# Kernel optimization log

Hardware: AMD Instinct MI355X
Metric: run time of the kernel (lower is better)

Reference implementation:

```python
import jax, jax.numpy as jnp
import numpy as np

N, T, F, H = 50000, 8, 128, 128
E = 800000


def setup_inputs() -> dict:
    key = jax.random.key(0)
    ks = jax.random.split(key, 10)
    s = 1.0 / np.sqrt(H)
    return {
        "node_features": jax.random.normal(ks[0], (T, N, F), jnp.float32),
        "edge_index": jax.random.randint(ks[1], (T, 2, E), 0, N),
        "W1": jax.random.normal(ks[2], (F, H), jnp.float32) * s,
        "b1": jnp.zeros((H,), jnp.float32),
        "W2": jax.random.normal(ks[3], (H, H), jnp.float32) * s,
        "b2": jnp.zeros((H,), jnp.float32),
        "W_ih": jax.random.uniform(ks[4], (4 * H, H), jnp.float32, -s, s),
        "W_hh": jax.random.uniform(ks[5], (4 * H, H), jnp.float32, -s, s),
        "b_ih": jax.random.uniform(ks[6], (4 * H,), jnp.float32, -s, s),
        "b_hh": jax.random.uniform(ks[7], (4 * H,), jnp.float32, -s, s),
    }


def gcn_layer(x, src, dst, W, b):
    """PyG GCNConv: add self loops, symmetric D^-1/2 (A+I) D^-1/2 normalization."""
    n = x.shape[0]
    h = x @ W  # [N, H]
    deg = jnp.zeros((n,), x.dtype).at[dst].add(1.0) + 1.0  # degree incl. self loop
    dinv = jax.lax.rsqrt(deg)
    norm = (dinv[src] * dinv[dst])[:, None]  # per-edge norm
    msg = h[src] * norm  # [E, H] gather + scale
    agg = jax.ops.segment_sum(msg, dst, num_segments=n)  # scatter-add at targets
    agg = agg + h * (dinv * dinv)[:, None]  # self-loop contribution
    return agg + b


def reference(node_features, edge_index, W1, b1, W2, b2, W_ih, W_hh, b_ih, b_hh):
    # per-timestep 2-layer GCN (dropout in eval mode -> identity)
    def step_gnn(_, xe):
        x, ei = xe
        src, dst = ei[0], ei[1]
        h = jax.nn.relu(gcn_layer(x, src, dst, W1, b1))
        h = jax.nn.relu(gcn_layer(h, src, dst, W2, b2))
        return None, h

    _, embs = jax.lax.scan(step_gnn, None, (node_features, edge_index))  # [T, N, H]

    # single-layer LSTM over T, batch dim = N; pytorch gate order i,f,g,o
    def lstm_step(carry, x_t):
        h, c = carry
        gates = x_t @ W_ih.T + h @ W_hh.T + b_ih + b_hh
        i, f, g, o = jnp.split(gates, 4, axis=-1)
        c = jax.nn.sigmoid(f) * c + jax.nn.sigmoid(i) * jnp.tanh(g)
        h = jax.nn.sigmoid(o) * jnp.tanh(c)
        return (h, c), None

    h0 = jnp.zeros((N, H), node_features.dtype)
    (h_last, _), _ = jax.lax.scan(lstm_step, (h0, h0), embs)
    return h_last  # [N, H] = lstm_out[:, -1, :]
```

## Files before the change

### kernel.cpp

```cpp
#include <hip/hip_runtime.h>
#include <cstdint>
#include <cstddef>

#define NN 50000
#define TT 8
#define FF 128
#define HH 128
#define EE 800000

#define NBUCK 782
#define NB 128
#define CHUNK 6250

typedef __attribute__((ext_vector_type(8))) short bf16x8;
typedef __attribute__((ext_vector_type(4))) float f32x4;
typedef unsigned int uint;
typedef unsigned short ushort;

__device__ __forceinline__ float sigmoidf(float x) { return 1.0f / (1.0f + expf(-x)); }

__device__ __forceinline__ ushort f2bf_rne(float x) {
    uint u = __float_as_uint(x);
    uint r = (u + 0x7FFFu + ((u >> 16) & 1u)) >> 16;
    return (ushort)r;
}
__device__ __forceinline__ float bf2f(ushort b) { return __uint_as_float(((uint)b) << 16); }
__device__ __forceinline__ void split1(float x, ushort& hi, ushort& lo) {
    ushort h = f2bf_rne(x);
    hi = h;
    lo = f2bf_rne(x - bf2f(h));
}


__global__ __launch_bounds__(256) void bin_hist(const int* __restrict__ ei,
                                                int* __restrict__ histG) {
    __shared__ int hist[NBUCK];
    const int tid = threadIdx.x;
    const int blk = blockIdx.x, t = blockIdx.y;
    for (int i = tid; i < NBUCK; i += 256) hist[i] = 0;
    __syncthreads();
    const int* dst = ei + (size_t)t * 2 * EE + EE;
    const int base = blk * CHUNK;
    for (int i = tid; i < CHUNK; i += 256) atomicAdd(&hist[dst[base + i] >> 6], 1);
    __syncthreads();
    int* hg = histG + (size_t)t * NBUCK * NB;
    for (int i = tid; i < NBUCK; i += 256) hg[i * NB + blk] = hist[i];
}

__global__ __launch_bounds__(256) void scan_bins(int* __restrict__ histG,
                                                 int* __restrict__ bOffs) {
    __shared__ int sums[256];
    const int t = blockIdx.x;
    int* hg = histG + (size_t)t * NBUCK * NB;
    int* bo = bOffs + (size_t)t * (NBUCK + 1);
    const int tid = threadIdx.x;
    const int SZ = NBUCK * NB;
    const int chunk = (SZ + 255) / 256;
    const int b = tid * chunk, e = min(b + chunk, SZ);
    int s = 0;
    for (int i = b; i < e; ++i) s += hg[i];
    sums[tid] = s;
    __syncthreads();
    for (int o = 1; o < 256; o <<= 1) {
        int v = 0;
        if (tid >= o) v = sums[tid - o];
        __syncthreads();
        if (tid >= o) sums[tid] += v;
        __syncthreads();
    }
    int pre = (tid == 0) ? 0 : sums[tid - 1];
    for (int i = b; i < e; ++i) {
        int v = hg[i];
        hg[i] = pre;
        if ((i & (NB - 1)) == 0) bo[i / NB] = pre;
        pre += v;
    }
    if (tid == 255) bo[NBUCK] = pre;
}

__global__ __launch_bounds__(256) void bin_scatter(const int* __restrict__ ei,
                                                   const int* __restrict__ histG,
                                                   uint* __restrict__ binned) {
    __shared__ int cur[NBUCK];
    const int tid = threadIdx.x;
    const int blk = blockIdx.x, t = blockIdx.y;
    const int* hg = histG + (size_t)t * NBUCK * NB;
    for (int i = tid; i < NBUCK; i += 256) cur[i] = hg[i * NB + blk];
    __syncthreads();
    const int* src = ei + (size_t)t * 2 * EE;
    const int* dst = src + EE;
    uint* bn = binned + (size_t)t * EE;
    const int base = blk * CHUNK;
    for (int i = tid; i < CHUNK; i += 256) {
        const int e = base + i;
        const int d = dst[e];
        const int s = src[e];
        const int pos = atomicAdd(&cur[d >> 6], 1);
        bn[pos] = ((uint)(d & 63) << 16) | (uint)s;
    }
}

__global__ __launch_bounds__(256) void bucket_csr(const uint* __restrict__ binned,
                                                  const int* __restrict__ bOffs,
                                                  int* __restrict__ sorted,
                                                  int* __restrict__ offs,
                                                  float* __restrict__ dinv) {
    __shared__ int cnt[64];
    __shared__ int base[64];
    const int tid = threadIdx.x;
    const int buck = blockIdx.x, t = blockIdx.y;
    if (tid < 64) cnt[tid] = 0;
    __syncthreads();
    const int* bo = bOffs + (size_t)t * (NBUCK + 1);
    const uint* bn = binned + (size_t)t * EE;
    const int e0 = bo[buck], e1 = bo[buck + 1];
    for (int e = e0 + tid; e < e1; e += 256) atomicAdd(&cnt[bn[e] >> 16], 1);
    __syncthreads();
    if (tid == 0) {
        int pre = e0;
#pragma unroll
        for (int i = 0; i < 64; ++i) { base[i] = pre; pre += cnt[i]; }
    }
    __syncthreads();
    if (tid < 64) {
        const int d = buck * 64 + tid;
        if (d < NN) {
            offs[(size_t)t * (NN + 1) + d] = base[tid];
            dinv[(size_t)t * NN + d] = rsqrtf((float)(cnt[tid] + 1));
        }
        cnt[tid] = 0;
    }
    __syncthreads();
    int* so = sorted + (size_t)t * EE;
    for (int e = e0 + tid; e < e1; e += 256) {
        const uint p = bn[e];
        const int dl = p >> 16;
        const int pos = base[dl] + atomicAdd(&cnt[dl], 1);
        so[pos] = (int)(p & 0xFFFF);
    }
    if (buck == 0 && tid == 0) offs[(size_t)t * (NN + 1) + NN] = EE;
}

__global__ void prep_w_gcn(const float* __restrict__ W, ushort* __restrict__ oh,
                           ushort* __restrict__ ol) {
    const int bx = blockIdx.x;
    const int kc5 = bx >> 3, q = bx & 7;
    const int l = threadIdx.x;
    const int n = q * 16 + (l & 15);
    const int kb = kc5 * 32 + (l >> 4) * 8;
    const size_t o = ((size_t)bx * 64 + l) * 8;
#pragma unroll
    for (int j = 0; j < 8; ++j) {
        float v = W[(size_t)(kb + j) * 128 + n];
        split1(v, oh[o + j], ol[o + j]);
    }
}

__global__ void prep_w_lstm(const float* __restrict__ W, ushort* __restrict__ oh,
                            ushort* __restrict__ ol) {
    const int bx = blockIdx.x;
    const int kc5 = bx >> 5, q = bx & 31;
    const int l = threadIdx.x;
    const int c15 = l & 15;
    const int g = q & 3, kk = q >> 2;
    const int srow = g * 128 + kk * 16 + c15;
    const int kb = kc5 * 32 + (l >> 4) * 8;
    const size_t o = ((size_t)bx * 64 + l) * 8;
#pragma unroll
    for (int j = 0; j < 8; ++j) {
        float v = W[(size_t)srow * 128 + kb + j];
        split1(v, oh[o + j], ol[o + j]);
    }
}

__global__ void prep_bc(const float* __restrict__ bih, const float* __restrict__ bhh,
                        float* __restrict__ bcp) {
    const int cp = threadIdx.x;
    const int c15 = cp & 15, q = cp >> 4;
    const int g = q & 3, kk = q >> 2;
    const int srow = g * 128 + kk * 16 + c15;
    bcp[cp] = bih[srow] + bhh[srow];
}

__global__ __launch_bounds__(256) void gemm_gcn_mfma(const float* __restrict__ A,
                                                     const ushort* __restrict__ Wfh,
                                                     const ushort* __restrict__ Wfl,
                                                     const float* __restrict__ dinv,
                                                     float* __restrict__ C, int M) {
    __shared__ ushort Ah[64][40];
    __shared__ ushort Al[64][40];
    const int tid = threadIdx.x;
    const int lane = tid & 63;
    const int w = tid >> 6;
    const int wm = w >> 1, wn = w & 1;
    const int l15 = lane & 15, l4 = lane >> 4;
    const int m0 = blockIdx.x * 64;

    f32x4 acc[2][4];
#pragma unroll
    for (int i = 0; i < 2; ++i)
#pragma unroll
        for (int j = 0; j < 4; ++j) acc[i][j] = (f32x4){0.f, 0.f, 0.f, 0.f};

    const int srow = tid >> 2;
    const int sseg = tid & 3;
    const bool aval = (m0 + srow) < M;
    const float* aptr = A + (size_t)(m0 + srow) * 128 + sseg * 8;

    for (int kc5 = 0; kc5 < 4; ++kc5) {
        float4 v0 = {0.f, 0.f, 0.f, 0.f}, v1 = {0.f, 0.f, 0.f, 0.f};
        if (aval) {
            v0 = *(const float4*)(aptr + kc5 * 32);
            v1 = *(const float4*)(aptr + kc5 * 32 + 4);
        }
        union { uint4 u; ushort s[8]; } ph, pl;
        split1(v0.x, ph.s[0], pl.s[0]); split1(v0.y, ph.s[1], pl.s[1]);
        split1(v0.z, ph.s[2], pl.s[2]); split1(v0.w, ph.s[3], pl.s[3]);
        split1(v1.x, ph.s[4], pl.s[4]); split1(v1.y, ph.s[5], pl.s[5]);
        split1(v1.z, ph.s[6], pl.s[6]); split1(v1.w, ph.s[7], pl.s[7]);
        *(uint4*)&Ah[srow][sseg * 8] = ph.u;
        *(uint4*)&Al[srow][sseg * 8] = pl.u;
        __syncthreads();

        bf16x8 bh[4], bl[4];
#pragma unroll
        for (int nf = 0; nf < 4; ++nf) {
            const size_t o = ((size_t)(kc5 * 8 + wn * 4 + nf) * 64 + lane) * 8;
            bh[nf] = *(const bf16x8*)(Wfh + o);
            bl[nf] = *(const bf16x8*)(Wfl + o);
        }
        bf16x8 ahf[2], alf[2];
#pragma unroll
        for (int mf = 0; mf < 2; ++mf) {
            ahf[mf] = *(const bf16x8*)&Ah[wm * 32 + mf * 16 + l15][l4 * 8];
            alf[mf] = *(const bf16x8*)&Al[wm * 32 + mf * 16 + l15][l4 * 8];
        }
#pragma unroll
        for (int mf = 0; mf < 2; ++mf)
#pragma unroll
            for (int nf = 0; nf < 4; ++nf) {
                acc[mf][nf] = __builtin_amdgcn_mfma_f32_16x16x32_bf16(ahf[mf], bh[nf], acc[mf][nf], 0, 0, 0);
                acc[mf][nf] = __builtin_amdgcn_mfma_f32_16x16x32_bf16(ahf[mf], bl[nf], acc[mf][nf], 0, 0, 0);
                acc[mf][nf] = __builtin_amdgcn_mfma_f32_16x16x32_bf16(alf[mf], bh[nf], acc[mf][nf], 0, 0, 0);
            }
        __syncthreads();
    }

#pragma unroll
    for (int mf = 0; mf < 2; ++mf)
#pragma unroll
        for (int r = 0; r < 4; ++r) {
            const int row = m0 + wm * 32 + mf * 16 + l4 * 4 + r;
            if (row < M) {
                const float d = dinv[row];
                float* cp = C + (size_t)row * 128 + wn * 64 + l15;
#pragma unroll
                for (int nf = 0; nf < 4; ++nf) cp[nf * 16] = acc[mf][nf][r] * d;
            }
        }
}

__global__ __launch_bounds__(256) void gemm_frag(const ushort* __restrict__ Xh,
                                                 const ushort* __restrict__ Xl,
                                                 const ushort* __restrict__ Wfh,
                                                 const ushort* __restrict__ Wfl,
                                                 const float* __restrict__ dinv,
                                                 float* __restrict__ C, int M) {
    const int tid = threadIdx.x;
    const int lane = tid & 63;
    const int w = tid >> 6;
    const int wm = w >> 1, wn = w & 1;
    const int l15 = lane & 15, l4 = lane >> 4;
    const int m0 = blockIdx.x * 64;

    f32x4 acc[2][4];
#pragma unroll
    for (int i = 0; i < 2; ++i)
#pragma unroll
        for (int j = 0; j < 4; ++j) acc[i][j] = (f32x4){0.f, 0.f, 0.f, 0.f};

    size_t abase[2];
#pragma unroll
    for (int mf = 0; mf < 2; ++mf)
        abase[mf] = (size_t)(m0 + wm * 32 + mf * 16 + l15) * 128 + l4 * 8;

#pragma unroll
    for (int kc5 = 0; kc5 < 4; ++kc5) {
        bf16x8 ahf[2], alf[2];
#pragma unroll
        for (int mf = 0; mf < 2; ++mf) {
            ahf[mf] = *(const bf16x8*)(Xh + abase[mf] + kc5 * 32);
            alf[mf] = *(const bf16x8*)(Xl + abase[mf] + kc5 * 32);
        }
#pragma unroll
        for (int nf = 0; nf < 4; ++nf) {
            const size_t o = ((size_t)(kc5 * 8 + wn * 4 + nf) * 64 + lane) * 8;
            const bf16x8 bh = *(const bf16x8*)(Wfh + o);
            const bf16x8 bl = *(const bf16x8*)(Wfl + o);
#pragma unroll
            for (int mf = 0; mf < 2; ++mf) {
                acc[mf][nf] = __builtin_amdgcn_mfma_f32_16x16x32_bf16(ahf[mf], bh, acc[mf][nf], 0, 0, 0);
                acc[mf][nf] = __builtin_amdgcn_mfma_f32_16x16x32_bf16(ahf[mf], bl, acc[mf][nf], 0, 0, 0);
                acc[mf][nf] = __builtin_amdgcn_mfma_f32_16x16x32_bf16(alf[mf], bh, acc[mf][nf], 0, 0, 0);
            }
        }
    }

#pragma unroll
    for (int mf = 0; mf < 2; ++mf)
#pragma unroll
        for (int r = 0; r < 4; ++r) {
            const int row = m0 + wm * 32 + mf * 16 + l4 * 4 + r;
            if (row < M) {
                const float d = dinv[row];
                float* cp = C + (size_t)row * 128 + wn * 64 + l15;
#pragma unroll
                for (int nf = 0; nf < 4; ++nf) cp[nf * 16] = acc[mf][nf][r] * d;
            }
        }
}

__global__ __launch_bounds__(256) void aggregate_q(const float* __restrict__ hs,
                                                   const int* __restrict__ offs,
                                                   const int* __restrict__ sorted,
                                                   const float* __restrict__ dinv,
                                                   const float* __restrict__ bias,
                                                   ushort* __restrict__ outh,
                                                   ushort* __restrict__ outl, int n) {
    const int lane = threadIdx.x & 63;
    const int qt = lane >> 4, li = lane & 15;
    const int wave = (blockIdx.x * blockDim.x + threadIdx.x) >> 6;
    const int nwaves = (gridDim.x * blockDim.x) >> 6;
    for (int d = wave; d < n; d += nwaves) {
        const int e0 = offs[d], e1 = offs[d + 1];
        float4 a0 = {0, 0, 0, 0}, b0 = {0, 0, 0, 0};
        float4 a1 = {0, 0, 0, 0}, b1 = {0, 0, 0, 0};
        const int fb = li * 8;
        for (int e = e0; e < e1; e += 8) {
            const int sl = ((lane < 8) && (e + lane < e1)) ? sorted[e + lane] : 0;
            const int s0 = __shfl(sl, qt);
            const int s1 = __shfl(sl, qt + 4);
            if (e + qt < e1) {
                const float4 v0 = *(const float4*)&hs[(size_t)s0 * 128 + fb];
                const float4 v1 = *(const float4*)&hs[(size_t)s0 * 128 + fb + 4];
                a0.x += v0.x; a0.y += v0.y; a0.z += v0.z; a0.w += v0.w;
                b0.x += v1.x; b0.y += v1.y; b0.z += v1.z; b0.w += v1.w;
            }
            if (e + qt + 4 < e1) {
                const float4 v0 = *(const float4*)&hs[(size_t)s1 * 128 + fb];
                const float4 v1 = *(const float4*)&hs[(size_t)s1 * 128 + fb + 4];
                a1.x += v0.x; a1.y += v0.y; a1.z += v0.z; a1.w += v0.w;
                b1.x += v1.x; b1.y += v1.y; b1.z += v1.z; b1.w += v1.w;
            }
        }
        a0.x += a1.x; a0.y += a1.y; a0.z += a1.z; a0.w += a1.w;
        b0.x += b1.x; b0.y += b1.y; b0.z += b1.z; b0.w += b1.w;
#pragma unroll
        for (int m = 16; m <= 32; m <<= 1) {
            a0.x += __shfl_xor(a0.x, m); a0.y += __shfl_xor(a0.y, m);
            a0.z += __shfl_xor(a0.z, m); a0.w += __shfl_xor(a0.w, m);
            b0.x += __shfl_xor(b0.x, m); b0.y += __shfl_xor(b0.y, m);
            b0.z += __shfl_xor(b0.z, m); b0.w += __shfl_xor(b0.w, m);
        }

        const float di = dinv[d];
        const float4 s0 = *(const float4*)&hs[(size_t)d * 128 + fb];
        const float4 s1 = *(const float4*)&hs[(size_t)d * 128 + fb + 4];
        const float4 c0 = *(const float4*)&bias[fb];
        const float4 c1 = *(const float4*)&bias[fb + 4];
        float o[8];
        o[0] = fmaxf(di * (a0.x + s0.x) + c0.x, 0.f);
        o[1] = fmaxf(di * (a0.y + s0.y) + c0.y, 0.f);
        o[2] = fmaxf(di * (a0.z + s0.z) + c0.z, 0.f);
        o[3] = fmaxf(di * (a0.w + s0.w) + c0.w, 0.f);
        o[4] = fmaxf(di * (b0.x + s1.x) + c1.x, 0.f);
        o[5] = fmaxf(di * (b0.y + s1.y) + c1.y, 0.f);
        o[6] = fmaxf(di * (b0.z + s1.z) + c1.z, 0.f);
        o[7] = fmaxf(di * (b0.w + s1.w) + c1.w, 0.f);
        ushort hh[8], ll[8];
#pragma unroll
        for (int j = 0; j < 8; ++j) split1(o[j], hh[j], ll[j]);
        if (qt == 0) {
            ushort4 p0 = {hh[0], hh[1], hh[2], hh[3]};
            ushort4 p1 = {hh[4], hh[5], hh[6], hh[7]};
            *(ushort4*)&outh[(size_t)d * 128 + fb] = p0;
            *(ushort4*)&outh[(size_t)d * 128 + fb + 4] = p1;
        } else if (qt == 1) {
            ushort4 p0 = {ll[0], ll[1], ll[2], ll[3]};
            ushort4 p1 = {ll[4], ll[5], ll[6], ll[7]};
            *(ushort4*)&outl[(size_t)d * 128 + fb] = p0;
            *(ushort4*)&outl[(size_t)d * 128 + fb + 4] = p1;
        }
    }
}

__global__ __launch_bounds__(512) void lstm_frag(const ushort* __restrict__ Xh,
                                                 const ushort* __restrict__ Xl,
                                                 const ushort* __restrict__ Hinh,
                                                 const ushort* __restrict__ Hinl,
                                                 ushort* __restrict__ Houth,
                                                 ushort* __restrict__ Houtl,
                                                 float* __restrict__ hout,
                                                 float* __restrict__ c,
                                                 const ushort* __restrict__ Wihfh,
                                                 const ushort* __restrict__ Wihfl,
                                                 const ushort* __restrict__ Whhfh,
                                                 const ushort* __restrict__ Whhfl,
                                                 const float* __restrict__ bcp, int M) {
    const int tid = threadIdx.x;
    const int lane = tid & 63;
    const int w = tid >> 6;
    const int wm = w >> 2, wn = w & 3;
    const int l15 = lane & 15, l4 = lane >> 4;
    const int m0 = blockIdx.x * 64;

    f32x4 acc[2][8];
#pragma unroll
    for (int i = 0; i < 2; ++i)
#pragma unroll
        for (int j = 0; j < 8; ++j) acc[i][j] = (f32x4){0.f, 0.f, 0.f, 0.f};

    size_t abase[2];
#pragma unroll
    for (int mf = 0; mf < 2; ++mf)
        abase[mf] = (size_t)(m0 + wm * 32 + mf * 16 + l15) * 128 + l4 * 8;

#pragma unroll
    for (int halfK = 0; halfK < 2; ++halfK) {
        const ushort* Ah = halfK ? Hinh : Xh;
        const ushort* Al = halfK ? Hinl : Xl;
        const ushort* Bfh = halfK ? Whhfh : Wihfh;
        const ushort* Bfl = halfK ? Whhfl : Wihfl;
#pragma unroll
        for (int kc5 = 0; kc5 < 4; ++kc5) {
            bf16x8 ahf[2], alf[2];
#pragma unroll
            for (int mf = 0; mf < 2; ++mf) {
                ahf[mf] = *(const bf16x8*)(Ah + abase[mf] + kc5 * 32);
                alf[mf] = *(const bf16x8*)(Al + abase[mf] + kc5 * 32);
            }
#pragma unroll
            for (int nf = 0; nf < 8; ++nf) {
                const size_t o = ((size_t)(kc5 * 32 + wn * 8 + nf) * 64 + lane) * 8;
                const bf16x8 bh = *(const bf16x8*)(Bfh + o);
                const bf16x8 bl = *(const bf16x8*)(Bfl + o);
#pragma unroll
                for (int mf = 0; mf < 2; ++mf) {
                    acc[mf][nf] = __builtin_amdgcn_mfma_f32_16x16x32_bf16(ahf[mf], bh, acc[mf][nf], 0, 0, 0);
                    acc[mf][nf] = __builtin_amdgcn_mfma_f32_16x16x32_bf16(ahf[mf], bl, acc[mf][nf], 0, 0, 0);
                    acc[mf][nf] = __builtin_amdgcn_mfma_f32_16x16x32_bf16(alf[mf], bh, acc[mf][nf], 0, 0, 0);
                }
            }
        }
    }

    float bb[8];
#pragma unroll
    for (int nf = 0; nf < 8; ++nf) bb[nf] = bcp[l15 + 16 * (wn * 8 + nf)];
#pragma unroll
    for (int mf = 0; mf < 2; ++mf)
#pragma unroll
        for (int r = 0; r < 4; ++r) {
            const int row = m0 + wm * 32 + mf * 16 + l4 * 4 + r;
            if (row >= M) continue;
#pragma unroll
            for (int kl = 0; kl < 2; ++kl) {
                const float gi = acc[mf][kl * 4 + 0][r] + bb[kl * 4 + 0];
                const float gf = acc[mf][kl * 4 + 1][r] + bb[kl * 4 + 1];
                const float gg = acc[mf][kl * 4 + 2][r] + bb[kl * 4 + 2];
                const float go = acc[mf][kl * 4 + 3][r] + bb[kl * 4 + 3];
                const int k = (2 * wn + kl) * 16 + l15;
                const size_t idx = (size_t)row * 128 + k;
                const float cn = sigmoidf(gf) * c[idx] + sigmoidf(gi) * tanhf(gg);
                const float hn = sigmoidf(go) * tanhf(cn);
                c[idx] = cn;
                hout[idx] = hn;
                ushort hh, hl;
                split1(hn, hh, hl);
                Houth[idx] = hh;
                Houtl[idx] = hl;
            }
        }
}

extern "C" void kernel_launch(void* const* d_in, const int* in_sizes, int n_in,
                              void* d_out, int out_size, void* d_ws, size_t ws_size,
                              hipStream_t stream) {
    const float* nf  = (const float*)d_in[0];
    const int*   ei  = (const int*)d_in[1];
    const float* W1  = (const float*)d_in[2];
    const float* b1  = (const float*)d_in[3];
    const float* W2  = (const float*)d_in[4];
    const float* b2  = (const float*)d_in[5];
    const float* Wih = (const float*)d_in[6];
    const float* Whh = (const float*)d_in[7];
    const float* bih = (const float*)d_in[8];
    const float* bhh = (const float*)d_in[9];
    float* h = (float*)d_out;

    const size_t AL = 256;
    auto rnd = [&](size_t b) { return (b + AL - 1) & ~(AL - 1); };
    const size_t sz_feat  = (size_t)NN * 128 * 4;
    const size_t sz_plane = (size_t)NN * 128 * 2;
    const size_t need = rnd(sz_feat) * 2
                      + rnd(sz_plane) * 6
                      + rnd((size_t)TT * EE * 4) * 2
                      + rnd((size_t)TT * NBUCK * NB * 4)
                      + rnd((size_t)TT * (NBUCK + 1) * 4)
                      + rnd((size_t)TT * (NN + 1) * 4)
                      + rnd((size_t)TT * NN * 4)
                      + rnd((size_t)128 * 128 * 2) * 4
                      + rnd((size_t)512 * 128 * 2) * 4
                      + rnd(512 * 4);
    if (ws_size < need) return;

    char* ws = (char*)d_ws;
    size_t off = 0;
    auto alloc = [&](size_t bytes) -> void* {
        void* p = ws + off;
        off += rnd(bytes);
        return p;
    };
    float*  hs     = (float*)alloc(sz_feat);
    float*  c      = (float*)alloc(sz_feat);
    ushort* xh     = (ushort*)alloc(sz_plane);
    ushort* xl     = (ushort*)alloc(sz_plane);
    ushort* hp0h   = (ushort*)alloc(sz_plane);
    ushort* hp0l   = (ushort*)alloc(sz_plane);
    ushort* hp1h   = (ushort*)alloc(sz_plane);
    ushort* hp1l   = (ushort*)alloc(sz_plane);
    uint*   binned = (uint*)alloc((size_t)TT * EE * 4);
    int*    sorted = (int*)alloc((size_t)TT * EE * 4);
    int*    histG  = (int*)alloc((size_t)TT * NBUCK * NB * 4);
    int*    bOffs  = (int*)alloc((size_t)TT * (NBUCK + 1) * 4);
    int*    offs   = (int*)alloc((size_t)TT * (NN + 1) * 4);
    float*  dinv   = (float*)alloc((size_t)TT * NN * 4);
    ushort* wf1h   = (ushort*)alloc((size_t)128 * 128 * 2);
    ushort* wf1l   = (ushort*)alloc((size_t)128 * 128 * 2);
    ushort* wf2h   = (ushort*)alloc((size_t)128 * 128 * 2);
    ushort* wf2l   = (ushort*)alloc((size_t)128 * 128 * 2);
    ushort* wihfh  = (ushort*)alloc((size_t)512 * 128 * 2);
    ushort* wihfl  = (ushort*)alloc((size_t)512 * 128 * 2);
    ushort* whhfh  = (ushort*)alloc((size_t)512 * 128 * 2);
    ushort* whhfl  = (ushort*)alloc((size_t)512 * 128 * 2);
    float*  bcp    = (float*)alloc(512 * 4);

    hipMemsetAsync(c, 0, sz_feat, stream);
    hipMemsetAsync(hp0h, 0, sz_plane, stream);
    hipMemsetAsync(hp0l, 0, sz_plane, stream);

    bin_hist<<<dim3(NB, TT), 256, 0, stream>>>(ei, histG);
    scan_bins<<<TT, 256, 0, stream>>>(histG, bOffs);
    bin_scatter<<<dim3(NB, TT), 256, 0, stream>>>(ei, histG, binned);
    bucket_csr<<<dim3(NBUCK, TT), 256, 0, stream>>>(binned, bOffs, sorted, offs, dinv);

    prep_w_gcn<<<32, 64, 0, stream>>>(W1, wf1h, wf1l);
    prep_w_gcn<<<32, 64, 0, stream>>>(W2, wf2h, wf2l);
    prep_w_lstm<<<128, 64, 0, stream>>>(Wih, wihfh, wihfl);
    prep_w_lstm<<<128, 64, 0, stream>>>(Whh, whhfh, whhfl);
    prep_bc<<<1, 512, 0, stream>>>(bih, bhh, bcp);

    const int gm64 = (NN + 63) / 64;
    const int gagg = (NN * 64) / 256;

    for (int t = 0; t < TT; ++t) {
        const float* x = nf + (size_t)t * NN * FF;
        const float* dv = dinv + (size_t)t * NN;
        const int* of = offs + (size_t)t * (NN + 1);
        const int* so = sorted + (size_t)t * EE;

        gemm_gcn_mfma<<<gm64, 256, 0, stream>>>(x, wf1h, wf1l, dv, hs, NN);
        aggregate_q<<<gagg, 256, 0, stream>>>(hs, of, so, dv, b1, xh, xl, NN);
        gemm_frag<<<gm64, 256, 0, stream>>>(xh, xl, wf2h, wf2l, dv, hs, NN);
        aggregate_q<<<gagg, 256, 0, stream>>>(hs, of, so, dv, b2, xh, xl, NN);

        const ushort* hinh = (t & 1) ? hp1h : hp0h;
        const ushort* hinl = (t & 1) ? hp1l : hp0l;
        ushort* houth = (t & 1) ? hp0h : hp1h;
        ushort* houtl = (t & 1) ? hp0l : hp1l;
        lstm_frag<<<gm64, 512, 0, stream>>>(xh, xl, hinh, hinl, houth, houtl, h, c,
                                            wihfh, wihfl, whhfh, whhfl, bcp, NN);
    }
}
```

Before: 2.710 ms.

## Split serial histogram scan into parallel reduce, scan, and per-bucket prefix kernels

Replaces the single scan_bins kernel with three steps. Each block handles one timestep there, and every thread serially walks about 390 histogram entries. The new path has wave-per-bucket shuffle reductions for bucket totals, a small scan over 782 bucket totals, and a wave-level shuffle prefix that writes per-block offsets in place. This spreads the previously serialized scan across many waves, at the cost of two extra launches and a small extra buffer.

```diff
diff --git a/kernel.cpp b/kernel.cpp
--- a/kernel.cpp
+++ b/kernel.cpp
@@ -47,18 +47,31 @@
     for (int i = tid; i < NBUCK; i += 256) hg[i * NB + blk] = hist[i];
 }
 
-__global__ __launch_bounds__(256) void scan_bins(int* __restrict__ histG,
+__global__ __launch_bounds__(256) void bucket_tot(const int* __restrict__ histG,
+                                                  int* __restrict__ btot) {
+    const int t = blockIdx.y;
+    const int wv = threadIdx.x >> 6;
+    const int lane = threadIdx.x & 63;
+    const int buck = blockIdx.x * 4 + wv;
+    if (buck >= NBUCK) return;
+    const int* hg = histG + (size_t)t * NBUCK * NB + (size_t)buck * NB;
+    int s = hg[lane] + hg[lane + 64];
+#pragma unroll
+    for (int m = 1; m < 64; m <<= 1) s += __shfl_xor(s, m);
+    if (lane == 0) btot[t * NBUCK + buck] = s;
+}
+
+__global__ __launch_bounds__(256) void scan_btot(const int* __restrict__ btot,
                                                  int* __restrict__ bOffs) {
     __shared__ int sums[256];
     const int t = blockIdx.x;
-    int* hg = histG + (size_t)t * NBUCK * NB;
+    const int* bt = btot + t * NBUCK;
     int* bo = bOffs + (size_t)t * (NBUCK + 1);
     const int tid = threadIdx.x;
-    const int SZ = NBUCK * NB;
-    const int chunk = (SZ + 255) / 256;
-    const int b = tid * chunk, e = min(b + chunk, SZ);
+    const int chunk = (NBUCK + 255) / 256;
+    const int b = tid * chunk, e = min(b + chunk, NBUCK);
     int s = 0;
-    for (int i = b; i < e; ++i) s += hg[i];
+    for (int i = b; i < e; ++i) s += bt[i];
     sums[tid] = s;
     __syncthreads();
     for (int o = 1; o < 256; o <<= 1) {
@@ -69,13 +82,29 @@
         __syncthreads();
     }
     int pre = (tid == 0) ? 0 : sums[tid - 1];
-    for (int i = b; i < e; ++i) {
-        int v = hg[i];
-        hg[i] = pre;
-        if ((i & (NB - 1)) == 0) bo[i / NB] = pre;
-        pre += v;
-    }
-    if (tid == 255) bo[NBUCK] = pre;
+    for (int i = b; i < e; ++i) { bo[i] = pre; pre += bt[i]; }
+    if (tid == 255) bo[NBUCK] = EE;
+}
+
+__global__ __launch_bounds__(256) void block_prefix(int* __restrict__ histG,
+                                                    const int* __restrict__ bOffs) {
+    const int t = blockIdx.y;
+    const int wv = threadIdx.x >> 6;
+    const int lane = threadIdx.x & 63;
+    const int buck = blockIdx.x * 4 + wv;
+    if (buck >= NBUCK) return;
+    int* hg = histG + (size_t)t * NBUCK * NB + (size_t)buck * NB;
+    const int base = bOffs[(size_t)t * (NBUCK + 1) + buck];
+    const int a = hg[lane * 2], b = hg[lane * 2 + 1];
+    int s = a + b;
+#pragma unroll
+    for (int o = 1; o < 64; o <<= 1) {
+        const int v = __shfl_up(s, o);
+        if (lane >= o) s += v;
+    }
+    const int excl = s - (a + b);
+    hg[lane * 2]     = base + excl;
+    hg[lane * 2 + 1] = base + excl + a;
 }
 
 __global__ __launch_bounds__(256) void bin_scatter(const int* __restrict__ ei,
@@ -506,6 +535,7 @@
                       + rnd(sz_plane) * 6
                       + rnd((size_t)TT * EE * 4) * 2
                       + rnd((size_t)TT * NBUCK * NB * 4)
+                      + rnd((size_t)TT * NBUCK * 4)
                       + rnd((size_t)TT * (NBUCK + 1) * 4)
                       + rnd((size_t)TT * (NN + 1) * 4)
                       + rnd((size_t)TT * NN * 4)
@@ -532,6 +562,7 @@
     uint*   binned = (uint*)alloc((size_t)TT * EE * 4);
     int*    sorted = (int*)alloc((size_t)TT * EE * 4);
     int*    histG  = (int*)alloc((size_t)TT * NBUCK * NB * 4);
+    int*    btot   = (int*)alloc((size_t)TT * NBUCK * 4);
     int*    bOffs  = (int*)alloc((size_t)TT * (NBUCK + 1) * 4);
     int*    offs   = (int*)alloc((size_t)TT * (NN + 1) * 4);
     float*  dinv   = (float*)alloc((size_t)TT * NN * 4);
@@ -549,8 +580,11 @@
     hipMemsetAsync(hp0h, 0, sz_plane, stream);
     hipMemsetAsync(hp0l, 0, sz_plane, stream);
 
+    const int gb4 = (NBUCK + 3) / 4;
     bin_hist<<<dim3(NB, TT), 256, 0, stream>>>(ei, histG);
-    scan_bins<<<TT, 256, 0, stream>>>(histG, bOffs);
+    bucket_tot<<<dim3(gb4, TT), 256, 0, stream>>>(histG, btot);
+    scan_btot<<<TT, 256, 0, stream>>>(btot, bOffs);
+    block_prefix<<<dim3(gb4, TT), 256, 0, stream>>>(histG, bOffs);
     bin_scatter<<<dim3(NB, TT), 256, 0, stream>>>(ei, histG, binned);
     bucket_csr<<<dim3(NBUCK, TT), 256, 0, stream>>>(binned, bOffs, sorted, offs, dinv);
 
```

New measurement: 2.560 ms. 5.5% less time.
